# Performance work log

Hardware: AMD Instinct MI355X
Metric: run time of the kernel (lower is better)

## Reference

```python
import jax, jax.numpy as jnp
import numpy as np

N = 50000
E = 1600000
IN = 128
HID = 128
OUT = 64
NEG_SLOPE = 0.2  # DGL GATConv default leaky_relu slope


def _gat_layer(h, src, dst, W, al, ar, b, res=None, act=True):
    """DGL GATConv layer on an edge-list graph.
    h: [N, F_in]; W: [F_in, H*D]; al, ar, b: [H, D]; res: None | [N,H,D].
    Returns [N, H, D].
    """
    H, D = al.shape
    f = (h @ W).reshape(N, H, D)                      # fc projection
    el = jnp.sum(f * al, axis=-1)                     # [N, H]
    er = jnp.sum(f * ar, axis=-1)                     # [N, H]
    e = jax.nn.leaky_relu(el[src] + er[dst], NEG_SLOPE)  # [E, H]
    # edge softmax over incoming edges of each dst node
    m = jax.ops.segment_max(e, dst, num_segments=N)   # [N, H]
    ex = jnp.exp(e - m[dst])                          # [E, H]
    s = jax.ops.segment_sum(ex, dst, num_segments=N)  # [N, H]
    alpha = ex / s[dst]                               # [E, H]
    msg = f[src] * alpha[..., None]                   # [E, H, D]
    rst = jax.ops.segment_sum(msg, dst, num_segments=N)  # [N, H, D]
    if res is not None:
        rst = rst + res
    rst = rst + b                                     # bias [H, D] broadcast
    if act:
        rst = jax.nn.elu(rst)
    return rst


def setup_inputs() -> dict:
    key = jax.random.key(0)
    ks = jax.random.split(key, 16)
    x = jax.random.normal(ks[0], (N, IN), dtype=jnp.float32)
    src = jax.random.randint(ks[1], (E,), 0, N)
    dst = jax.random.randint(ks[2], (E,), 0, N)
    sc = 0.05
    # layer 0: IN -> 8 heads x 16, no residual, elu
    W0 = jax.random.normal(ks[3], (IN, 8 * 16), dtype=jnp.float32) * sc
    al0 = jax.random.normal(ks[4], (8, 16), dtype=jnp.float32) * sc
    ar0 = jax.random.normal(ks[5], (8, 16), dtype=jnp.float32) * sc
    b0 = jnp.zeros((8, 16), dtype=jnp.float32)
    # layer 1: HID -> 8 heads x 16, identity residual (HID == 8*16), elu
    W1 = jax.random.normal(ks[6], (HID, 8 * 16), dtype=jnp.float32) * sc
    al1 = jax.random.normal(ks[7], (8, 16), dtype=jnp.float32) * sc
    ar1 = jax.random.normal(ks[8], (8, 16), dtype=jnp.float32) * sc
    b1 = jnp.zeros((8, 16), dtype=jnp.float32)
    # layer 2: HID -> 1 head x 64, linear residual (128 != 64), no act
    W2 = jax.random.normal(ks[9], (HID, 1 * OUT), dtype=jnp.float32) * sc
    al2 = jax.random.normal(ks[10], (1, OUT), dtype=jnp.float32) * sc
    ar2 = jax.random.normal(ks[11], (1, OUT), dtype=jnp.float32) * sc
    b2 = jnp.zeros((1, OUT), dtype=jnp.float32)
    resW2 = jax.random.normal(ks[12], (HID, 1 * OUT), dtype=jnp.float32) * sc
    return {"x": x, "src": src, "dst": dst,
            "W0": W0, "al0": al0, "ar0": ar0, "b0": b0,
            "W1": W1, "al1": al1, "ar1": ar1, "b1": b1,
            "W2": W2, "al2": al2, "ar2": ar2, "b2": b2,
            "resW2": resW2}


def reference(x, src, dst, W0, al0, ar0, b0, W1, al1, ar1, b1,
              W2, al2, ar2, b2, resW2):
    # layer 0: no residual, elu, flatten heads (dropout=0)
    h = _gat_layer(x, src, dst, W0, al0, ar0, b0, res=None, act=True)
    h = h.reshape(N, -1)  # [N, 128]
    # layer 1: identity residual, elu, flatten heads
    res1 = h.reshape(N, 8, 16)
    h = _gat_layer(h, src, dst, W1, al1, ar1, b1, res=res1, act=True)
    h = h.reshape(N, -1)  # [N, 128]
    # layer 2: linear residual, no activation, mean over heads
    res2 = (h @ resW2).reshape(N, 1, OUT)
    h = _gat_layer(h, src, dst, W2, al2, ar2, b2, res=res2, act=False)
    return h.mean(axis=1)  # [N, 64]
```

## Files before the change

kernel.cpp:

```cpp
#include <hip/hip_runtime.h>
#include <hip/hip_fp16.h>
#include <math.h>


#define GN 50000
#define GE 1600000
#define NB 391
#define NBLK_A 512
#define CHUNK 3125

typedef _Float16 half8 __attribute__((ext_vector_type(8)));
typedef float f32x4 __attribute__((ext_vector_type(4)));


__global__ __launch_bounds__(256) void bucketA(const int* __restrict__ dst, int* __restrict__ cnt) {
    __shared__ int hist[NB];
    for (int i = threadIdx.x; i < NB; i += 256) hist[i] = 0;
    __syncthreads();
    int b = blockIdx.x;
    int beg = b * CHUNK, end = beg + CHUNK;
    for (int i = beg + threadIdx.x; i < end; i += 256)
        atomicAdd(&hist[dst[i] >> 7], 1);
    __syncthreads();
    for (int k = threadIdx.x; k < NB; k += 256)
        cnt[k * NBLK_A + b] = hist[k];
}

__global__ __launch_bounds__(512) void bucketB(int* __restrict__ cnt, int* __restrict__ tot) {
    __shared__ int s[512];
    int k = blockIdx.x, t = threadIdx.x;
    int* row = cnt + k * NBLK_A;
    s[t] = row[t];
    __syncthreads();
    for (int ofs = 1; ofs < 512; ofs <<= 1) {
        int v = (t >= ofs) ? s[t - ofs] : 0;
        __syncthreads();
        s[t] += v;
        __syncthreads();
    }
    row[t] = (t == 0) ? 0 : s[t - 1];
    if (t == 511) tot[k] = s[511];
}

__global__ __launch_bounds__(512) void bucketB2(const int* __restrict__ tot, int* __restrict__ base,
                                                int* __restrict__ offs) {
    __shared__ int s[512];
    int t = threadIdx.x;
    s[t] = (t < NB) ? tot[t] : 0;
    __syncthreads();
    for (int ofs = 1; ofs < 512; ofs <<= 1) {
        int v = (t >= ofs) ? s[t - ofs] : 0;
        __syncthreads();
        s[t] += v;
        __syncthreads();
    }
    if (t <= NB) base[t] = (t == 0) ? 0 : s[t - 1];
    if (t == 0) offs[GN] = GE;
}

__global__ __launch_bounds__(256) void bucketC(const int* __restrict__ src, const int* __restrict__ dst,
                                               const int* __restrict__ cnt, const int* __restrict__ base,
                                               unsigned* __restrict__ ebuf) {
    __shared__ int cur[NB];
    int b = blockIdx.x;
    for (int k = threadIdx.x; k < NB; k += 256)
        cur[k] = base[k] + cnt[k * NBLK_A + b];
    __syncthreads();
    int beg = b * CHUNK, end = beg + CHUNK;
    for (int i = beg + threadIdx.x; i < end; i += 256) {
        int d = dst[i];
        int pos = atomicAdd(&cur[d >> 7], 1);
        ebuf[pos] = (unsigned)src[i] | ((unsigned)(d & 127) << 16);
    }
}

__global__ __launch_bounds__(256) void bucketD(const unsigned* __restrict__ ebuf, const int* __restrict__ base,
                                               int* __restrict__ offs, int* __restrict__ csrc) {
    __shared__ int hist[128], pre[128], cur[128];
    int k = blockIdx.x, t = threadIdx.x;
    if (t < 128) hist[t] = 0;
    __syncthreads();
    int lo = base[k], hi = base[k + 1];
    for (int i = lo + t; i < hi; i += 256)
        atomicAdd(&hist[ebuf[i] >> 16], 1);
    __syncthreads();
    if (t < 128) pre[t] = hist[t];
    __syncthreads();
    for (int ofs = 1; ofs < 128; ofs <<= 1) {
        int v = 0;
        if (t < 128 && t >= ofs) v = pre[t - ofs];
        __syncthreads();
        if (t < 128) pre[t] += v;
        __syncthreads();
    }
    if (t < 128) {
        int excl = (t == 0) ? 0 : pre[t - 1];
        cur[t] = lo + excl;
        int node = (k << 7) + t;
        if (node < GN) offs[node] = lo + excl;
    }
    __syncthreads();
    for (int i = lo + t; i < hi; i += 256) {
        unsigned v = ebuf[i];
        int pos = atomicAdd(&cur[v >> 16], 1);
        csrc[pos] = (int)(v & 0xFFFFu);
    }
}


__global__ __launch_bounds__(256) void wt_ker(const float* __restrict__ W, _Float16* __restrict__ WT, int N) {
    int i = blockIdx.x * 256 + threadIdx.x;
    if (i >= N * 128) return;
    int n = i >> 7, k = i & 127;
    WT[i] = (_Float16)W[k * N + n];
}

__global__ __launch_bounds__(256) void cvt_ker(const float4* __restrict__ X, __half2* __restrict__ Y, int n4) {
    int i = blockIdx.x * 256 + threadIdx.x;
    if (i >= n4) return;
    float4 v = X[i];
    Y[i * 2]     = __floats2half2_rn(v.x, v.y);
    Y[i * 2 + 1] = __floats2half2_rn(v.z, v.w);
}


template <int NT>
__global__ __launch_bounds__(256) void gemm_mfma(const _Float16* __restrict__ A,
                                                 const _Float16* __restrict__ WT,
                                                 _Float16* __restrict__ C, int nrows) {
    const int N = NT * 16;
    int wave = threadIdx.x >> 6;
    int lane = threadIdx.x & 63;
    int quad = lane >> 4;
    int l16 = lane & 15;
    int m = blockIdx.x * 64 + wave * 16 + l16;
    int mc = (m < nrows) ? m : (nrows - 1);
    const _Float16* ap = A + (size_t)mc * 128 + quad * 8;
    half8 a[4];
    #pragma unroll
    for (int kk = 0; kk < 4; ++kk) a[kk] = *(const half8*)(ap + kk * 32);
    f32x4 acc[NT];
    #pragma unroll
    for (int nt = 0; nt < NT; ++nt) acc[nt] = (f32x4){0.f, 0.f, 0.f, 0.f};
    const _Float16* wp = WT + (size_t)l16 * 128 + quad * 8;
    #pragma unroll
    for (int nt = 0; nt < NT; ++nt) {
        #pragma unroll
        for (int kk = 0; kk < 4; ++kk) {
            half8 b = *(const half8*)(wp + nt * 16 * 128 + kk * 32);
            acc[nt] = __builtin_amdgcn_mfma_f32_16x16x32_f16(a[kk], b, acc[nt], 0, 0, 0);
        }
    }
    int row0 = blockIdx.x * 64 + wave * 16 + quad * 4;
    #pragma unroll
    for (int nt = 0; nt < NT; ++nt) {
        #pragma unroll
        for (int r = 0; r < 4; ++r) {
            int row = row0 + r;
            if (row < nrows) C[(size_t)row * N + nt * 16 + l16] = (_Float16)acc[nt][r];
        }
    }
}


template <int H, int D>
__global__ __launch_bounds__(256) void attn_ker(const __half* __restrict__ f, const float* __restrict__ al,
                                                const float* __restrict__ ar, float* __restrict__ el,
                                                float* __restrict__ er, int total) {
    int i = blockIdx.x * 256 + threadIdx.x;
    if (i >= total) return;
    int h = i % H;
    const __half2* fp = (const __half2*)(f + (size_t)i * D);
    const float2* alp = (const float2*)(al + h * D);
    const float2* arp = (const float2*)(ar + h * D);
    float sl = 0.f, sr = 0.f;
    #pragma unroll
    for (int d = 0; d < D / 2; ++d) {
        float2 fv = __half22float2(fp[d]);
        float2 av = alp[d];
        float2 rv = arp[d];
        sl += fv.x * av.x + fv.y * av.y;
        sr += fv.x * rv.x + fv.y * rv.y;
    }
    el[i] = sl;
    er[i] = sr;
}


__global__ __launch_bounds__(256) void agg_multi(const int* __restrict__ offs, const int* __restrict__ csrc,
                                                 const __half2* __restrict__ fh, const float* __restrict__ el,
                                                 const float* __restrict__ er, const float* __restrict__ bias,
                                                 const __half2* __restrict__ resid, __half2* __restrict__ out,
                                                 int n) {
    int node = blockIdx.x * 4 + (threadIdx.x >> 6);
    int lane = threadIdx.x & 63;
    if (node >= n) return;
    int h = lane >> 3;
    float ern_w = er[node * 8 + (lane & 7)];
    int beg = offs[node], end = offs[node + 1];
    float ssum = 0.f, ax = 0.f, ay = 0.f;
    for (int idx = beg; idx < end; idx += 8) {
        int s[8];
        #pragma unroll
        for (int j = 0; j < 8; ++j) {
            int t = idx + j;
            s[j] = csrc[t < end ? t : end - 1];
        }
        int me = idx + (lane >> 3);
        int swe = csrc[me < end ? me : end - 1];
        float e = el[swe * 8 + (lane & 7)] + ern_w;
        e = fmaxf(e, 0.2f * e);
        float we = __expf(e);
        if (me >= end) we = 0.f;
        __half2 q[8];
        #pragma unroll
        for (int j = 0; j < 8; ++j) q[j] = fh[s[j] * 64 + lane];
        #pragma unroll
        for (int j = 0; j < 8; ++j) {
            float w = __shfl(we, (j << 3) + h, 64);
            float2 g = __half22float2(q[j]);
            ssum += w;
            ax += w * g.x;
            ay += w * g.y;
        }
    }
    float inv = (ssum > 0.f) ? (1.0f / ssum) : 0.f;
    int c = lane * 2;
    float ox = ax * inv + bias[c];
    float oy = ay * inv + bias[c + 1];
    if (resid) {
        float2 rv = __half22float2(resid[node * 64 + lane]);
        ox += rv.x;
        oy += rv.y;
    }
    ox = (ox > 0.f) ? ox : expm1f(ox);
    oy = (oy > 0.f) ? oy : expm1f(oy);
    out[node * 64 + lane] = __floats2half2_rn(ox, oy);
}

__global__ __launch_bounds__(256) void agg_single(const int* __restrict__ offs, const int* __restrict__ csrc,
                                                  const __half* __restrict__ fh, const float* __restrict__ el,
                                                  const float* __restrict__ er, const float* __restrict__ bias,
                                                  const __half* __restrict__ resid, float* __restrict__ out,
                                                  int n) {
    int node = blockIdx.x * 4 + (threadIdx.x >> 6);
    int lane = threadIdx.x & 63;
    if (node >= n) return;
    float ern = er[node];
    int beg = offs[node], end = offs[node + 1];
    float ssum = 0.f, acc = 0.f;
    for (int idx = beg; idx < end; idx += 8) {
        int s[8];
        #pragma unroll
        for (int j = 0; j < 8; ++j) {
            int t = idx + j;
            s[j] = csrc[t < end ? t : end - 1];
        }
        int me = idx + (lane & 7);
        int swe = csrc[me < end ? me : end - 1];
        float e = el[swe] + ern;
        e = fmaxf(e, 0.2f * e);
        float we = __expf(e);
        if (me >= end) we = 0.f;
        __half q[8];
        #pragma unroll
        for (int j = 0; j < 8; ++j) q[j] = fh[s[j] * 64 + lane];
        #pragma unroll
        for (int j = 0; j < 8; ++j) {
            float w = __shfl(we, (lane & 56) + j, 64);
            ssum += w;
            acc += w * __half2float(q[j]);
        }
    }
    float inv = (ssum > 0.f) ? (1.0f / ssum) : 0.f;
    out[node * 64 + lane] = acc * inv + bias[lane] + __half2float(resid[node * 64 + lane]);
}


extern "C" void kernel_launch(void* const* d_in, const int* in_sizes, int n_in,
                              void* d_out, int out_size, void* d_ws, size_t ws_size,
                              hipStream_t stream) {
    const float* x     = (const float*)d_in[0];
    const int*   src   = (const int*)d_in[1];
    const int*   dst   = (const int*)d_in[2];
    const float* W0    = (const float*)d_in[3];
    const float* al0   = (const float*)d_in[4];
    const float* ar0   = (const float*)d_in[5];
    const float* b0    = (const float*)d_in[6];
    const float* W1    = (const float*)d_in[7];
    const float* al1   = (const float*)d_in[8];
    const float* ar1   = (const float*)d_in[9];
    const float* b1    = (const float*)d_in[10];
    const float* W2    = (const float*)d_in[11];
    const float* al2   = (const float*)d_in[12];
    const float* ar2   = (const float*)d_in[13];
    const float* b2    = (const float*)d_in[14];
    const float* resW2 = (const float*)d_in[15];
    float* out = (float*)d_out;

    char* w = (char*)d_ws;
    auto alloc = [&](size_t bytes) {
        char* p = w;
        w += (bytes + 255) & ~(size_t)255;
        return p;
    };
    int*      base  = (int*)alloc((size_t)(NB + 1) * 4);
    int*      offs  = (int*)alloc((size_t)(GN + 1) * 4);
    int*      csrc  = (int*)alloc((size_t)GE * 4);
    _Float16* fbuf  = (_Float16*)alloc((size_t)GN * 128 * 2);
    float*    elb   = (float*)alloc((size_t)GN * 8 * 4);
    float*    erb   = (float*)alloc((size_t)GN * 8 * 4);
    _Float16* x16   = (_Float16*)alloc((size_t)GN * 128 * 2);
    _Float16* hA    = (_Float16*)alloc((size_t)GN * 128 * 2);
    _Float16* hB    = (_Float16*)alloc((size_t)GN * 128 * 2);
    _Float16* res2  = (_Float16*)alloc((size_t)GN * 64 * 2);
    _Float16* w0t   = (_Float16*)alloc(128 * 128 * 2);
    _Float16* w1t   = (_Float16*)alloc(128 * 128 * 2);
    _Float16* w2t   = (_Float16*)alloc(64 * 128 * 2);
    _Float16* rw2t  = (_Float16*)alloc(64 * 128 * 2);

    int*      cnt  = (int*)hA;
    int*      tot  = (int*)hA + NB * NBLK_A;
    unsigned* ebuf = (unsigned*)hB;

    bucketA<<<NBLK_A, 256, 0, stream>>>(dst, cnt);
    bucketB<<<NB, 512, 0, stream>>>(cnt, tot);
    bucketB2<<<1, 512, 0, stream>>>(tot, base, offs);
    bucketC<<<NBLK_A, 256, 0, stream>>>(src, dst, cnt, base, ebuf);
    bucketD<<<NB, 256, 0, stream>>>(ebuf, base, offs, csrc);

    wt_ker<<<(128 * 128 + 255) / 256, 256, 0, stream>>>(W0, w0t, 128);
    wt_ker<<<(128 * 128 + 255) / 256, 256, 0, stream>>>(W1, w1t, 128);
    wt_ker<<<(64 * 128 + 255) / 256, 256, 0, stream>>>(W2, w2t, 64);
    wt_ker<<<(64 * 128 + 255) / 256, 256, 0, stream>>>(resW2, rw2t, 64);
    cvt_ker<<<(GN * 32 + 255) / 256, 256, 0, stream>>>((const float4*)x, (__half2*)x16, GN * 32);

    dim3 gblk(256);
    int gemmGrid = (GN + 63) / 64;
    int aggGrid = (GN + 3) / 4;

    gemm_mfma<8><<<gemmGrid, gblk, 0, stream>>>(x16, w0t, fbuf, GN);
    attn_ker<8, 16><<<(GN * 8 + 255) / 256, gblk, 0, stream>>>((const __half*)fbuf, al0, ar0, elb, erb, GN * 8);
    agg_multi<<<aggGrid, gblk, 0, stream>>>(offs, csrc, (const __half2*)fbuf, elb, erb, b0,
                                            nullptr, (__half2*)hA, GN);

    gemm_mfma<8><<<gemmGrid, gblk, 0, stream>>>(hA, w1t, fbuf, GN);
    attn_ker<8, 16><<<(GN * 8 + 255) / 256, gblk, 0, stream>>>((const __half*)fbuf, al1, ar1, elb, erb, GN * 8);
    agg_multi<<<aggGrid, gblk, 0, stream>>>(offs, csrc, (const __half2*)fbuf, elb, erb, b1,
                                            (const __half2*)hA, (__half2*)hB, GN);

    gemm_mfma<4><<<gemmGrid, gblk, 0, stream>>>(hB, w2t, fbuf, GN);
    gemm_mfma<4><<<gemmGrid, gblk, 0, stream>>>(hB, rw2t, res2, GN);
    attn_ker<1, 64><<<(GN + 255) / 256, gblk, 0, stream>>>((const __half*)fbuf, al2, ar2, elb, erb, GN);
    agg_single<<<aggGrid, gblk, 0, stream>>>(offs, csrc, (const __half*)fbuf, elb, erb, b2,
                                             (const __half*)res2, out, GN);
}
```

Before: 415.4 us.

## Aggregate each node with 16 lanes and wide half8 gathers

Both aggregation kernels now give each destination node 16 threads instead of a full 64-lane wavefront, so one block handles 16 nodes instead of 4. Each thread loads 8 halves (or 4 for the single-head layer) per source row with vector loads, and computes its own attention weight directly rather than sharing it through cross-lane shuffles. Edges are unrolled by four with a scalar tail loop, which removes the padded clamped loads. The aim is fewer idle lanes on low-degree nodes, fewer shuffles and wider memory transactions. The cost is redundant el/csrc loads across lanes of the same node and more registers per thread.

After: 402.9 us. -3.0%, faster.

```diff
diff --git a/kernel.cpp b/kernel.cpp
--- a/kernel.cpp
+++ b/kernel.cpp
@@ -10,6 +10,7 @@
 #define CHUNK 3125
 
 typedef _Float16 half8 __attribute__((ext_vector_type(8)));
+typedef _Float16 half4v __attribute__((ext_vector_type(4)));
 typedef float f32x4 __attribute__((ext_vector_type(4)));
 
 
@@ -188,92 +189,121 @@
 
 
 __global__ __launch_bounds__(256) void agg_multi(const int* __restrict__ offs, const int* __restrict__ csrc,
-                                                 const __half2* __restrict__ fh, const float* __restrict__ el,
+                                                 const _Float16* __restrict__ fh, const float* __restrict__ el,
                                                  const float* __restrict__ er, const float* __restrict__ bias,
-                                                 const __half2* __restrict__ resid, __half2* __restrict__ out,
+                                                 const _Float16* __restrict__ resid, _Float16* __restrict__ out,
                                                  int n) {
-    int node = blockIdx.x * 4 + (threadIdx.x >> 6);
-    int lane = threadIdx.x & 63;
+    int node = blockIdx.x * 16 + (threadIdx.x >> 4);
+    int lg = threadIdx.x & 15;
     if (node >= n) return;
-    int h = lane >> 3;
-    float ern_w = er[node * 8 + (lane & 7)];
+    int head = lg >> 1;
+    float ern = er[node * 8 + head];
     int beg = offs[node], end = offs[node + 1];
-    float ssum = 0.f, ax = 0.f, ay = 0.f;
-    for (int idx = beg; idx < end; idx += 8) {
-        int s[8];
-        #pragma unroll
-        for (int j = 0; j < 8; ++j) {
-            int t = idx + j;
-            s[j] = csrc[t < end ? t : end - 1];
-        }
-        int me = idx + (lane >> 3);
-        int swe = csrc[me < end ? me : end - 1];
-        float e = el[swe * 8 + (lane & 7)] + ern_w;
-        e = fmaxf(e, 0.2f * e);
-        float we = __expf(e);
-        if (me >= end) we = 0.f;
-        __half2 q[8];
-        #pragma unroll
-        for (int j = 0; j < 8; ++j) q[j] = fh[s[j] * 64 + lane];
-        #pragma unroll
-        for (int j = 0; j < 8; ++j) {
-            float w = __shfl(we, (j << 3) + h, 64);
-            float2 g = __half22float2(q[j]);
-            ssum += w;
-            ax += w * g.x;
-            ay += w * g.y;
-        }
-    }
-    float inv = (ssum > 0.f) ? (1.0f / ssum) : 0.f;
-    int c = lane * 2;
-    float ox = ax * inv + bias[c];
-    float oy = ay * inv + bias[c + 1];
+    float acc[8] = {};
+    float ssum = 0.f;
+    int e = beg;
+    for (; e + 4 <= end; e += 4) {
+        int s0 = csrc[e], s1 = csrc[e + 1], s2 = csrc[e + 2], s3 = csrc[e + 3];
+        float e0 = el[s0 * 8 + head] + ern;
+        float e1 = el[s1 * 8 + head] + ern;
+        float e2 = el[s2 * 8 + head] + ern;
+        float e3 = el[s3 * 8 + head] + ern;
+        half8 q0 = *(const half8*)(fh + (size_t)s0 * 128 + lg * 8);
+        half8 q1 = *(const half8*)(fh + (size_t)s1 * 128 + lg * 8);
+        half8 q2 = *(const half8*)(fh + (size_t)s2 * 128 + lg * 8);
+        half8 q3 = *(const half8*)(fh + (size_t)s3 * 128 + lg * 8);
+        e0 = fmaxf(e0, 0.2f * e0);
+        e1 = fmaxf(e1, 0.2f * e1);
+        e2 = fmaxf(e2, 0.2f * e2);
+        e3 = fmaxf(e3, 0.2f * e3);
+        float w0 = __expf(e0), w1 = __expf(e1), w2 = __expf(e2), w3 = __expf(e3);
+        ssum += (w0 + w1) + (w2 + w3);
+        #pragma unroll
+        for (int j = 0; j < 8; ++j)
+            acc[j] += w0 * (float)q0[j] + w1 * (float)q1[j]
+                    + w2 * (float)q2[j] + w3 * (float)q3[j];
+    }
+    for (; e < end; ++e) {
+        int s = csrc[e];
+        float ev = el[s * 8 + head] + ern;
+        ev = fmaxf(ev, 0.2f * ev);
+        float w = __expf(ev);
+        half8 q = *(const half8*)(fh + (size_t)s * 128 + lg * 8);
+        ssum += w;
+        #pragma unroll
+        for (int j = 0; j < 8; ++j) acc[j] += w * (float)q[j];
+    }
+    float inv = (ssum > 0.f) ? 1.0f / ssum : 0.f;
+    float o[8];
+    #pragma unroll
+    for (int j = 0; j < 8; ++j) o[j] = acc[j] * inv + bias[lg * 8 + j];
     if (resid) {
-        float2 rv = __half22float2(resid[node * 64 + lane]);
-        ox += rv.x;
-        oy += rv.y;
-    }
-    ox = (ox > 0.f) ? ox : expm1f(ox);
-    oy = (oy > 0.f) ? oy : expm1f(oy);
-    out[node * 64 + lane] = __floats2half2_rn(ox, oy);
+        half8 r = *(const half8*)(resid + (size_t)node * 128 + lg * 8);
+        #pragma unroll
+        for (int j = 0; j < 8; ++j) o[j] += (float)r[j];
+    }
+    half8 ov;
+    #pragma unroll
+    for (int j = 0; j < 8; ++j) {
+        float v = o[j];
+        v = (v > 0.f) ? v : expm1f(v);
+        ov[j] = (_Float16)v;
+    }
+    *(half8*)(out + (size_t)node * 128 + lg * 8) = ov;
 }
 
 __global__ __launch_bounds__(256) void agg_single(const int* __restrict__ offs, const int* __restrict__ csrc,
-                                                  const __half* __restrict__ fh, const float* __restrict__ el,
+                                                  const _Float16* __restrict__ fh, const float* __restrict__ el,
                                                   const float* __restrict__ er, const float* __restrict__ bias,
-                                                  const __half* __restrict__ resid, float* __restrict__ out,
+                                                  const _Float16* __restrict__ resid, float* __restrict__ out,
                                                   int n) {
-    int node = blockIdx.x * 4 + (threadIdx.x >> 6);
-    int lane = threadIdx.x & 63;
+    int node = blockIdx.x * 16 + (threadIdx.x >> 4);
+    int lg = threadIdx.x & 15;
     if (node >= n) return;
     float ern = er[node];
     int beg = offs[node], end = offs[node + 1];
-    float ssum = 0.f, acc = 0.f;
-    for (int idx = beg; idx < end; idx += 8) {
-        int s[8];
-        #pragma unroll
-        for (int j = 0; j < 8; ++j) {
-            int t = idx + j;
-            s[j] = csrc[t < end ? t : end - 1];
-        }
-        int me = idx + (lane & 7);
-        int swe = csrc[me < end ? me : end - 1];
-        float e = el[swe] + ern;
-        e = fmaxf(e, 0.2f * e);
-        float we = __expf(e);
-        if (me >= end) we = 0.f;
-        __half q[8];
-        #pragma unroll
-        for (int j = 0; j < 8; ++j) q[j] = fh[s[j] * 64 + lane];
-        #pragma unroll
-        for (int j = 0; j < 8; ++j) {
-            float w = __shfl(we, (lane & 56) + j, 64);
-            ssum += w;
-            acc += w * __half2float(q[j]);
-        }
-    }
-    float inv = (ssum > 0.f) ? (1.0f / ssum) : 0.f;
-    out[node * 64 + lane] = acc * inv + bias[lane] + __half2float(resid[node * 64 + lane]);
+    float acc[4] = {};
+    float ssum = 0.f;
+    int e = beg;
+    for (; e + 4 <= end; e += 4) {
+        int s0 = csrc[e], s1 = csrc[e + 1], s2 = csrc[e + 2], s3 = csrc[e + 3];
+        float e0 = el[s0] + ern;
+        float e1 = el[s1] + ern;
+        float e2 = el[s2] + ern;
+        float e3 = el[s3] + ern;
+        half4v q0 = *(const half4v*)(fh + (size_t)s0 * 64 + lg * 4);
+        half4v q1 = *(const half4v*)(fh + (size_t)s1 * 64 + lg * 4);
+        half4v q2 = *(const half4v*)(fh + (size_t)s2 * 64 + lg * 4);
+        half4v q3 = *(const half4v*)(fh + (size_t)s3 * 64 + lg * 4);
+        e0 = fmaxf(e0, 0.2f * e0);
+        e1 = fmaxf(e1, 0.2f * e1);
+        e2 = fmaxf(e2, 0.2f * e2);
+        e3 = fmaxf(e3, 0.2f * e3);
+        float w0 = __expf(e0), w1 = __expf(e1), w2 = __expf(e2), w3 = __expf(e3);
+        ssum += (w0 + w1) + (w2 + w3);
+        #pragma unroll
+        for (int j = 0; j < 4; ++j)
+            acc[j] += w0 * (float)q0[j] + w1 * (float)q1[j]
+                    + w2 * (float)q2[j] + w3 * (float)q3[j];
+    }
+    for (; e < end; ++e) {
+        int s = csrc[e];
+        float ev = el[s] + ern;
+        ev = fmaxf(ev, 0.2f * ev);
+        float w = __expf(ev);
+        half4v q = *(const half4v*)(fh + (size_t)s * 64 + lg * 4);
+        ssum += w;
+        #pragma unroll
+        for (int j = 0; j < 4; ++j) acc[j] += w * (float)q[j];
+    }
+    float inv = (ssum > 0.f) ? 1.0f / ssum : 0.f;
+    half4v r = *(const half4v*)(resid + (size_t)node * 64 + lg * 4);
+    float4 o;
+    o.x = acc[0] * inv + bias[lg * 4 + 0] + (float)r[0];
+    o.y = acc[1] * inv + bias[lg * 4 + 1] + (float)r[1];
+    o.z = acc[2] * inv + bias[lg * 4 + 2] + (float)r[2];
+    o.w = acc[3] * inv + bias[lg * 4 + 3] + (float)r[3];
+    *(float4*)(out + (size_t)node * 64 + lg * 4) = o;
 }
 
 
@@ -337,21 +367,18 @@
 
     dim3 gblk(256);
     int gemmGrid = (GN + 63) / 64;
-    int aggGrid = (GN + 3) / 4;
+    int aggGrid = (GN + 15) / 16;
 
     gemm_mfma<8><<<gemmGrid, gblk, 0, stream>>>(x16, w0t, fbuf, GN);
     attn_ker<8, 16><<<(GN * 8 + 255) / 256, gblk, 0, stream>>>((const __half*)fbuf, al0, ar0, elb, erb, GN * 8);
-    agg_multi<<<aggGrid, gblk, 0, stream>>>(offs, csrc, (const __half2*)fbuf, elb, erb, b0,
-                                            nullptr, (__half2*)hA, GN);
+    agg_multi<<<aggGrid, gblk, 0, stream>>>(offs, csrc, fbuf, elb, erb, b0, nullptr, hA, GN);
 
     gemm_mfma<8><<<gemmGrid, gblk, 0, stream>>>(hA, w1t, fbuf, GN);
     attn_ker<8, 16><<<(GN * 8 + 255) / 256, gblk, 0, stream>>>((const __half*)fbuf, al1, ar1, elb, erb, GN * 8);
-    agg_multi<<<aggGrid, gblk, 0, stream>>>(offs, csrc, (const __half2*)fbuf, elb, erb, b1,
-                                            (const __half2*)hA, (__half2*)hB, GN);
+    agg_multi<<<aggGrid, gblk, 0, stream>>>(offs, csrc, fbuf, elb, erb, b1, hA, hB, GN);
 
     gemm_mfma<4><<<gemmGrid, gblk, 0, stream>>>(hB, w2t, fbuf, GN);
     gemm_mfma<4><<<gemmGrid, gblk, 0, stream>>>(hB, rw2t, res2, GN);
     attn_ker<1, 64><<<(GN + 255) / 256, gblk, 0, stream>>>((const __half*)fbuf, al2, ar2, elb, erb, GN);
-    agg_single<<<aggGrid, gblk, 0, stream>>>(offs, csrc, (const __half*)fbuf, elb, erb, b2,
-                                             (const __half*)res2, out, GN);
-}
+    agg_single<<<aggGrid, gblk, 0, stream>>>(offs, csrc, fbuf, elb, erb, b2, res2, out, GN);
+}
```
